# Optimization experiments

Measured on AMD Instinct MI355X. Metric: run time of the kernel, lower is better.

## Reference

```python
import jax, jax.numpy as jnp
import numpy as np

N_NODES = 100000
DEG = 16
N_EDGES = N_NODES * DEG
D_IN = 128
D_OUT = 128
N_BLK = 12500  # ceil(N_NODES/8) block-partition metadata (unused in math)


def setup_inputs() -> dict:
    key = jax.random.key(0)
    k_x, k_w, k_c = jax.random.split(key, 3)
    X = jax.random.normal(k_x, (N_NODES, D_IN), dtype=jnp.float32)
    weights = jax.random.normal(k_w, (D_IN, D_OUT), dtype=jnp.float32) / np.sqrt(D_OUT)
    # fixed-degree CSR graph
    row_pointers = (jnp.arange(N_NODES + 1, dtype=jnp.int32) * DEG)
    column_index = jax.random.randint(k_c, (N_EDGES,), 0, N_NODES, dtype=jnp.int32)
    # tensor-core tiling metadata: scheduling only, no effect on the math
    blockPartition = jnp.ones((N_BLK,), dtype=jnp.int32)
    edgeToColumn = jnp.zeros((N_EDGES,), dtype=jnp.int32)
    edgeToRow = jnp.zeros((N_EDGES,), dtype=jnp.int32)
    hybrid_type = jnp.zeros((N_BLK,), dtype=jnp.int32)
    row_nzr = jnp.zeros((N_BLK,), dtype=jnp.int32)
    col_nzr = jnp.zeros((N_EDGES,), dtype=jnp.int32)
    output = jnp.zeros((N_NODES, D_OUT), dtype=jnp.float32)
    return {
        "X": X, "weights": weights,
        "row_pointers": row_pointers, "column_index": column_index,
        "blockPartition": blockPartition, "edgeToColumn": edgeToColumn,
        "edgeToRow": edgeToRow, "hybrid_type": hybrid_type,
        "row_nzr": row_nzr, "col_nzr": col_nzr, "output": output,
    }


def reference(X, weights, row_pointers, column_index, blockPartition,
              edgeToColumn, edgeToRow, hybrid_type, row_nzr, col_nzr, output):
    n_nodes = X.shape[0]
    n_edges = column_index.shape[0]
    # row id of each edge from CSR row pointers (jit-safe)
    row_ids = jnp.searchsorted(row_pointers, jnp.arange(n_edges, dtype=row_pointers.dtype),
                               side="right").astype(jnp.int32) - 1
    # GIN sum aggregation: X_prime[r] = sum_{e: row(e)=r} X[col(e)]  (binary SpMM)
    gathered = X[column_index]                                   # [E, D]
    X_prime = jax.ops.segment_sum(gathered, row_ids, num_segments=n_nodes)
    # fused dense GEMM
    return X_prime @ weights
```

## Files before the change

### kernel.cpp

```cpp
#include <hip/hip_runtime.h>


#define NNODES 100000
#define DEG 16
#define D 128
#define MT 32
#define XPS 136

#define XB_BYTES (100000L * 128 * 2)
#define WT_BYTES (128L * 128 * 2)
#define WS_NEEDED (XB_BYTES + WT_BYTES)

typedef __attribute__((ext_vector_type(8))) short bf16x8;
typedef __attribute__((ext_vector_type(4))) float f32x4;

__device__ __forceinline__ unsigned short f2bf(float x) {
  union { float f; unsigned u; } v; v.f = x;
  unsigned r = v.u + 0x7FFFu + ((v.u >> 16) & 1u);
  return (unsigned short)(r >> 16);
}
__device__ __forceinline__ float bf2f(short s) {
  union { unsigned u; float f; } t;
  t.u = ((unsigned)(unsigned short)s) << 16;
  return t.f;
}

__global__ __launch_bounds__(256) void prep_wt(const float* __restrict__ W,
                                               unsigned short* __restrict__ Wt) {
  int t = blockIdx.x * 256 + threadIdx.x;
  int n = t >> 7, k = t & 127;
  Wt[n * D + k] = f2bf(W[k * D + n]);
}

__global__ __launch_bounds__(256) void prep_x(const float* __restrict__ X,
                                              unsigned short* __restrict__ Xb) {
  long t = (long)blockIdx.x * 256 + threadIdx.x;
  float4 v = ((const float4*)X)[t];
  ushort4 o;
  o.x = f2bf(v.x); o.y = f2bf(v.y); o.z = f2bf(v.z); o.w = f2bf(v.w);
  ((ushort4*)Xb)[t] = o;
}

__global__ __launch_bounds__(256, 4) void gin_fused_bf16(
    const unsigned short* __restrict__ Xb, const int* __restrict__ colidx,
    const unsigned short* __restrict__ Wt, float* __restrict__ out) {
  __shared__ __align__(16) unsigned short sXp[MT * XPS];
  __shared__ __align__(16) int sIdx[MT * DEG];

  const int tid  = threadIdx.x;
  const int wave = tid >> 6;
  const int lane = tid & 63;
  const long base_node = (long)blockIdx.x * MT;

  ((int2*)sIdx)[tid] = ((const int2*)(colidx + base_node * DEG))[tid];
  __syncthreads();

  const int q = lane >> 4;
  const int l = lane & 15;
  #pragma unroll
  for (int p = 0; p < 2; ++p) {
    int local = wave * 8 + p * 4 + q;
    int4 i4[4];
    #pragma unroll
    for (int t = 0; t < 4; ++t) i4[t] = ((const int4*)(sIdx + local * DEG))[t];
    int idx[16] = {i4[0].x, i4[0].y, i4[0].z, i4[0].w,
                   i4[1].x, i4[1].y, i4[1].z, i4[1].w,
                   i4[2].x, i4[2].y, i4[2].z, i4[2].w,
                   i4[3].x, i4[3].y, i4[3].z, i4[3].w};
    bf16x8 v[DEG];
    #pragma unroll
    for (int j = 0; j < DEG; ++j)
      v[j] = *(const bf16x8*)(Xb + (long)idx[j] * D + l * 8);
    __builtin_amdgcn_sched_barrier(0);
    float acc[8] = {0.f, 0.f, 0.f, 0.f, 0.f, 0.f, 0.f, 0.f};
    #pragma unroll
    for (int j = 0; j < DEG; ++j)
      #pragma unroll
      for (int e = 0; e < 8; ++e) acc[e] += bf2f(v[j][e]);
    bf16x8 o;
    #pragma unroll
    for (int e = 0; e < 8; ++e) o[e] = (short)f2bf(acc[e]);
    *(bf16x8*)(&sXp[local * XPS + l * 8]) = o;
  }
  __syncthreads();

  const int fr   = lane & 15;
  const int quad = lane >> 4;
  f32x4 acc[2][2] = {{{0.f,0.f,0.f,0.f},{0.f,0.f,0.f,0.f}},
                     {{0.f,0.f,0.f,0.f},{0.f,0.f,0.f,0.f}}};
  #pragma unroll
  for (int ks = 0; ks < 4; ++ks) {
    int k0 = ks * 32 + quad * 8;
    bf16x8 a0 = *(const bf16x8*)(&sXp[fr        * XPS + k0]);
    bf16x8 a1 = *(const bf16x8*)(&sXp[(16 + fr) * XPS + k0]);
    #pragma unroll
    for (int nt = 0; nt < 2; ++nt) {
      int n = (wave * 2 + nt) * 16 + fr;
      bf16x8 bfrag = *(const bf16x8*)(&Wt[n * D + k0]);
      acc[0][nt] = __builtin_amdgcn_mfma_f32_16x16x32_bf16(a0, bfrag, acc[0][nt], 0, 0, 0);
      acc[1][nt] = __builtin_amdgcn_mfma_f32_16x16x32_bf16(a1, bfrag, acc[1][nt], 0, 0, 0);
    }
  }

  #pragma unroll
  for (int mt = 0; mt < 2; ++mt)
    #pragma unroll
    for (int nt = 0; nt < 2; ++nt) {
      int col = (wave * 2 + nt) * 16 + fr;
      long rowbase = base_node + mt * 16 + quad * 4;
      #pragma unroll
      for (int r = 0; r < 4; ++r)
        out[(rowbase + r) * D + col] = acc[mt][nt][r];
    }
}

__global__ __launch_bounds__(256) void gin_fused_f32(
    const float* __restrict__ X, const int* __restrict__ colidx,
    const unsigned short* __restrict__ Wt, float* __restrict__ out) {
  __shared__ __align__(16) unsigned short sXp[MT * XPS];
  __shared__ int sIdx[MT * DEG];
  const int tid  = threadIdx.x;
  const int wave = tid >> 6;
  const int lane = tid & 63;
  const long base_node = (long)blockIdx.x * MT;
  ((int2*)sIdx)[tid] = ((const int2*)(colidx + base_node * DEG))[tid];
  __syncthreads();
  const int half = lane >> 5, l32 = lane & 31;
  const float4* X4 = (const float4*)X;
  #pragma unroll
  for (int p = 0; p < 4; ++p) {
    int local = wave * 8 + p * 2 + half;
    float4 acc = make_float4(0.f, 0.f, 0.f, 0.f);
    #pragma unroll
    for (int j = 0; j < DEG; ++j) {
      int c = sIdx[local * DEG + j];
      float4 v = X4[(long)c * (D / 4) + l32];
      acc.x += v.x; acc.y += v.y; acc.z += v.z; acc.w += v.w;
    }
    ushort4 b;
    b.x = f2bf(acc.x); b.y = f2bf(acc.y); b.z = f2bf(acc.z); b.w = f2bf(acc.w);
    *(ushort4*)(&sXp[local * XPS + l32 * 4]) = b;
  }
  __syncthreads();
  const int fr = lane & 15, quad = lane >> 4;
  f32x4 acc[2][2] = {{{0.f,0.f,0.f,0.f},{0.f,0.f,0.f,0.f}},
                     {{0.f,0.f,0.f,0.f},{0.f,0.f,0.f,0.f}}};
  #pragma unroll
  for (int ks = 0; ks < 4; ++ks) {
    int k0 = ks * 32 + quad * 8;
    bf16x8 a0 = *(const bf16x8*)(&sXp[fr        * XPS + k0]);
    bf16x8 a1 = *(const bf16x8*)(&sXp[(16 + fr) * XPS + k0]);
    #pragma unroll
    for (int nt = 0; nt < 2; ++nt) {
      int n = (wave * 2 + nt) * 16 + fr;
      bf16x8 bfrag = *(const bf16x8*)(&Wt[n * D + k0]);
      acc[0][nt] = __builtin_amdgcn_mfma_f32_16x16x32_bf16(a0, bfrag, acc[0][nt], 0, 0, 0);
      acc[1][nt] = __builtin_amdgcn_mfma_f32_16x16x32_bf16(a1, bfrag, acc[1][nt], 0, 0, 0);
    }
  }
  #pragma unroll
  for (int mt = 0; mt < 2; ++mt)
    #pragma unroll
    for (int nt = 0; nt < 2; ++nt) {
      int col = (wave * 2 + nt) * 16 + fr;
      long rowbase = base_node + mt * 16 + quad * 4;
      #pragma unroll
      for (int r = 0; r < 4; ++r)
        out[(rowbase + r) * D + col] = acc[mt][nt][r];
    }
}

extern "C" void kernel_launch(void* const* d_in, const int* in_sizes, int n_in,
                              void* d_out, int out_size, void* d_ws, size_t ws_size,
                              hipStream_t stream) {
  const float* X      = (const float*)d_in[0];
  const float* W      = (const float*)d_in[1];
  const int*   colidx = (const int*)d_in[3];
  float* out = (float*)d_out;

  if (ws_size >= (size_t)WS_NEEDED) {
    unsigned short* Xb = (unsigned short*)d_ws;
    unsigned short* Wt = (unsigned short*)((char*)d_ws + XB_BYTES);
    hipLaunchKernelGGL(prep_wt, dim3(64), dim3(256), 0, stream, W, Wt);
    hipLaunchKernelGGL(prep_x, dim3(12500), dim3(256), 0, stream, X, Xb);
    hipLaunchKernelGGL(gin_fused_bf16, dim3(NNODES / MT), dim3(256), 0, stream,
                       Xb, colidx, Wt, out);
  } else {
    unsigned short* Wt = (unsigned short*)d_ws;
    hipLaunchKernelGGL(prep_wt, dim3(64), dim3(256), 0, stream, W, Wt);
    hipLaunchKernelGGL(gin_fused_f32, dim3(NNODES / MT), dim3(256), 0, stream,
                       X, colidx, Wt, out);
  }
}
```

Measured before the change: 211.3 us.

## Merge X/W bf16 prep kernels and ring-buffer gather loads across both nodes

Fuses the two prep kernels (weight transpose-convert and X bf16 conversion) into one launch, removing one kernel launch and its tail. In the fused GIN kernel, the per-node gather (16 loads then sum, twice) becomes one 32-load stream over both nodes with an 8-deep register ring buffer. Loads for the next neighbours are issued while earlier ones are being summed, so the second node's loads no longer wait behind the first node's. Fewer live registers than 16 bf16x8 vectors may help occupancy, but the shallower prefetch depth lowers memory-level parallelism per wave.

Measured after the change: 209.0 us. Within noise of the previous version (-1.1%).

```diff
diff --git a/kernel.cpp b/kernel.cpp
--- a/kernel.cpp
+++ b/kernel.cpp
@@ -25,20 +25,23 @@
   return t.f;
 }
 
-__global__ __launch_bounds__(256) void prep_wt(const float* __restrict__ W,
-                                               unsigned short* __restrict__ Wt) {
-  int t = blockIdx.x * 256 + threadIdx.x;
-  int n = t >> 7, k = t & 127;
-  Wt[n * D + k] = f2bf(W[k * D + n]);
-}
-
-__global__ __launch_bounds__(256) void prep_x(const float* __restrict__ X,
-                                              unsigned short* __restrict__ Xb) {
-  long t = (long)blockIdx.x * 256 + threadIdx.x;
-  float4 v = ((const float4*)X)[t];
-  ushort4 o;
-  o.x = f2bf(v.x); o.y = f2bf(v.y); o.z = f2bf(v.z); o.w = f2bf(v.w);
-  ((ushort4*)Xb)[t] = o;
+__global__ __launch_bounds__(256) void prep_x_wt(const float* __restrict__ X,
+                                                 unsigned short* __restrict__ Xb,
+                                                 const float* __restrict__ W,
+                                                 unsigned short* __restrict__ Wt,
+                                                 int do_x) {
+  if (do_x) {
+    long t = (long)blockIdx.x * 256 + threadIdx.x;
+    float4 v = ((const float4*)X)[t];
+    ushort4 o;
+    o.x = f2bf(v.x); o.y = f2bf(v.y); o.z = f2bf(v.z); o.w = f2bf(v.w);
+    ((ushort4*)Xb)[t] = o;
+  }
+  if (blockIdx.x < 64) {
+    int u = blockIdx.x * 256 + threadIdx.x;
+    int n = u >> 7, k = u & 127;
+    Wt[n * D + k] = f2bf(W[k * D + n]);
+  }
 }
 
 __global__ __launch_bounds__(256, 4) void gin_fused_bf16(
@@ -57,37 +60,54 @@
 
   const int q = lane >> 4;
   const int l = lane & 15;
-  #pragma unroll
-  for (int p = 0; p < 2; ++p) {
-    int local = wave * 8 + p * 4 + q;
-    int4 i4[4];
-    #pragma unroll
-    for (int t = 0; t < 4; ++t) i4[t] = ((const int4*)(sIdx + local * DEG))[t];
-    int idx[16] = {i4[0].x, i4[0].y, i4[0].z, i4[0].w,
-                   i4[1].x, i4[1].y, i4[1].z, i4[1].w,
-                   i4[2].x, i4[2].y, i4[2].z, i4[2].w,
-                   i4[3].x, i4[3].y, i4[3].z, i4[3].w};
-    bf16x8 v[DEG];
-    #pragma unroll
-    for (int j = 0; j < DEG; ++j)
-      v[j] = *(const bf16x8*)(Xb + (long)idx[j] * D + l * 8);
-    __builtin_amdgcn_sched_barrier(0);
-    float acc[8] = {0.f, 0.f, 0.f, 0.f, 0.f, 0.f, 0.f, 0.f};
-    #pragma unroll
-    for (int j = 0; j < DEG; ++j)
+  const int localA = wave * 8 + q;
+  const int localB = wave * 8 + 4 + q;
+
+  int4 i4[8];
+  #pragma unroll
+  for (int t = 0; t < 4; ++t) i4[t]     = ((const int4*)(sIdx + localA * DEG))[t];
+  #pragma unroll
+  for (int t = 0; t < 4; ++t) i4[4 + t] = ((const int4*)(sIdx + localB * DEG))[t];
+  int idx[32] = {i4[0].x, i4[0].y, i4[0].z, i4[0].w,
+                 i4[1].x, i4[1].y, i4[1].z, i4[1].w,
+                 i4[2].x, i4[2].y, i4[2].z, i4[2].w,
+                 i4[3].x, i4[3].y, i4[3].z, i4[3].w,
+                 i4[4].x, i4[4].y, i4[4].z, i4[4].w,
+                 i4[5].x, i4[5].y, i4[5].z, i4[5].w,
+                 i4[6].x, i4[6].y, i4[6].z, i4[6].w,
+                 i4[7].x, i4[7].y, i4[7].z, i4[7].w};
+
+  const unsigned short* xb_l = Xb + l * 8;
+
+  bf16x8 v[8];
+  #pragma unroll
+  for (int j = 0; j < 8; ++j)
+    v[j] = *(const bf16x8*)(xb_l + ((long)idx[j] << 7));
+
+  float acc[8] = {0.f, 0.f, 0.f, 0.f, 0.f, 0.f, 0.f, 0.f};
+  #pragma unroll
+  for (int j = 0; j < 32; ++j) {
+    #pragma unroll
+    for (int e = 0; e < 8; ++e) acc[e] += bf2f(v[j & 7][e]);
+    if (j + 8 < 32)
+      v[j & 7] = *(const bf16x8*)(xb_l + ((long)idx[j + 8] << 7));
+    if (j == 15) {
+      bf16x8 oa;
       #pragma unroll
-      for (int e = 0; e < 8; ++e) acc[e] += bf2f(v[j][e]);
-    bf16x8 o;
-    #pragma unroll
-    for (int e = 0; e < 8; ++e) o[e] = (short)f2bf(acc[e]);
-    *(bf16x8*)(&sXp[local * XPS + l * 8]) = o;
-  }
+      for (int e = 0; e < 8; ++e) { oa[e] = (short)f2bf(acc[e]); acc[e] = 0.f; }
+      *(bf16x8*)(&sXp[localA * XPS + l * 8]) = oa;
+    }
+  }
+  bf16x8 ob;
+  #pragma unroll
+  for (int e = 0; e < 8; ++e) ob[e] = (short)f2bf(acc[e]);
+  *(bf16x8*)(&sXp[localB * XPS + l * 8]) = ob;
   __syncthreads();
 
   const int fr   = lane & 15;
   const int quad = lane >> 4;
-  f32x4 acc[2][2] = {{{0.f,0.f,0.f,0.f},{0.f,0.f,0.f,0.f}},
-                     {{0.f,0.f,0.f,0.f},{0.f,0.f,0.f,0.f}}};
+  f32x4 acc2[2][2] = {{{0.f,0.f,0.f,0.f},{0.f,0.f,0.f,0.f}},
+                      {{0.f,0.f,0.f,0.f},{0.f,0.f,0.f,0.f}}};
   #pragma unroll
   for (int ks = 0; ks < 4; ++ks) {
     int k0 = ks * 32 + quad * 8;
@@ -97,8 +117,8 @@
     for (int nt = 0; nt < 2; ++nt) {
       int n = (wave * 2 + nt) * 16 + fr;
       bf16x8 bfrag = *(const bf16x8*)(&Wt[n * D + k0]);
-      acc[0][nt] = __builtin_amdgcn_mfma_f32_16x16x32_bf16(a0, bfrag, acc[0][nt], 0, 0, 0);
-      acc[1][nt] = __builtin_amdgcn_mfma_f32_16x16x32_bf16(a1, bfrag, acc[1][nt], 0, 0, 0);
+      acc2[0][nt] = __builtin_amdgcn_mfma_f32_16x16x32_bf16(a0, bfrag, acc2[0][nt], 0, 0, 0);
+      acc2[1][nt] = __builtin_amdgcn_mfma_f32_16x16x32_bf16(a1, bfrag, acc2[1][nt], 0, 0, 0);
     }
   }
 
@@ -110,7 +130,7 @@
       long rowbase = base_node + mt * 16 + quad * 4;
       #pragma unroll
       for (int r = 0; r < 4; ++r)
-        out[(rowbase + r) * D + col] = acc[mt][nt][r];
+        out[(rowbase + r) * D + col] = acc2[mt][nt][r];
     }
 }
 
@@ -181,13 +201,14 @@
   if (ws_size >= (size_t)WS_NEEDED) {
     unsigned short* Xb = (unsigned short*)d_ws;
     unsigned short* Wt = (unsigned short*)((char*)d_ws + XB_BYTES);
-    hipLaunchKernelGGL(prep_wt, dim3(64), dim3(256), 0, stream, W, Wt);
-    hipLaunchKernelGGL(prep_x, dim3(12500), dim3(256), 0, stream, X, Xb);
+    hipLaunchKernelGGL(prep_x_wt, dim3(12500), dim3(256), 0, stream,
+                       X, Xb, W, Wt, 1);
     hipLaunchKernelGGL(gin_fused_bf16, dim3(NNODES / MT), dim3(256), 0, stream,
                        Xb, colidx, Wt, out);
   } else {
     unsigned short* Wt = (unsigned short*)d_ws;
-    hipLaunchKernelGGL(prep_wt, dim3(64), dim3(256), 0, stream, W, Wt);
+    hipLaunchKernelGGL(prep_x_wt, dim3(64), dim3(256), 0, stream,
+                       X, (unsigned short*)nullptr, W, Wt, 0);
     hipLaunchKernelGGL(gin_fused_f32, dim3(NNODES / MT), dim3(256), 0, stream,
                        X, colidx, Wt, out);
   }
```
